# Kernel optimization log

Measured on AMD Instinct MI355X. Metric: run time of the kernel, lower is better.

## Reference

```python
import jax, jax.numpy as jnp
import numpy as np


def _scan(x):
    # x: [B, C, D0, D1, D2] -> [B, 4, C, L] with L = D0*D1*D2
    B, C = x.shape[0], x.shape[1]
    x0 = x.reshape(B, C, -1)                          # row-major flatten of (D0,D1,D2)
    x1 = jnp.swapaxes(x, -2, -1).reshape(B, C, -1)    # swap last two spatial axes then flatten
    x2 = jnp.flip(x0, axis=-1)
    x3 = jnp.flip(x1, axis=-1)
    return jnp.stack([x0, x1, x2, x3], axis=1)        # [B, 4, C, L]


def setup_inputs() -> dict:
    key = jax.random.key(0)
    x = jax.random.normal(key, (2, 96, 32, 32, 32), dtype=jnp.float32)
    return {"x": x}


def reference(x) -> jnp.ndarray:
    # x: [B, C, I, J, K]
    xs_i = _scan(x)                                   # scan over (i, j, k)
    xs_j = _scan(jnp.transpose(x, (0, 1, 3, 4, 2)))   # b c i j k -> b c j k i
    xs_k = _scan(jnp.transpose(x, (0, 1, 4, 2, 3)))   # b c i j k -> b c k i j
    return jnp.concatenate([xs_i, xs_j, xs_k], axis=1)  # [B, 12, C, I*J*K]
```

## Files before the change

### kernel.cpp

```cpp
#include <hip/hip_runtime.h>

#define L 32768
#define NC 96
#define PL 4

typedef float f4 __attribute__((ext_vector_type(4)));


__global__ __launch_bounds__(256) void cross_scan3d(const float* __restrict__ in,
                                                    float* __restrict__ out) {
    __shared__ float lds[PL][32][33];

    const int bx   = blockIdx.x;
    const int type = bx & 1;
    const int bc   = bx >> 1;
    const int b    = bc / NC;
    const int c    = bc % NC;
    const int w0   = blockIdx.y * PL;
    const int tid  = threadIdx.x;

    const int row = tid >> 3;
    const int k4  = tid & 7;

    const f4* src4 = (const f4*)(in + (size_t)bc * L);

    const int sI = type ? 5 : 0;
    const int sT = type ? 4 : 1;
    const int sS = type ? 9 : 8;

    f4* oI  = (f4*)(out + ((size_t)(b*12 + sI    )*NC + c) * L);
    f4* oIf = (f4*)(out + ((size_t)(b*12 + sI + 2)*NC + c) * L);
    f4* oT  = (f4*)(out + ((size_t)(b*12 + sT    )*NC + c) * L);
    f4* oTf = (f4*)(out + ((size_t)(b*12 + sT + 2)*NC + c) * L);
    f4* oS  = (f4*)(out + ((size_t)(b*12 + sS    )*NC + c) * L);
    f4* oSf = (f4*)(out + ((size_t)(b*12 + sS + 2)*NC + c) * L);

    f4 v0, v1, v2, v3;
    #define LADDR(it) (type ? (row*256 + (w0+(it))*8 + k4) : ((w0+(it))*256 + row*8 + k4))
    v0 = src4[LADDR(0)]; v1 = src4[LADDR(1)]; v2 = src4[LADDR(2)]; v3 = src4[LADDR(3)];
    #undef LADDR

    #define STASH(p, V) \
        lds[p][row][k4*4+0] = V.x; lds[p][row][k4*4+1] = V.y; \
        lds[p][row][k4*4+2] = V.z; lds[p][row][k4*4+3] = V.w;
    STASH(0, v0) STASH(1, v1) STASH(2, v2) STASH(3, v3)
    #undef STASH

    __syncthreads();

    #pragma unroll
    for (int p = 0; p < PL; ++p) {
        const int gp = w0 + p;

        f4 a;
        a.x = lds[p][row][k4*4+0];
        a.y = lds[p][row][k4*4+1];
        a.z = lds[p][row][k4*4+2];
        a.w = lds[p][row][k4*4+3];

        f4 t;
        t.x = lds[p][k4*4+0][row];
        t.y = lds[p][k4*4+1][row];
        t.z = lds[p][k4*4+2][row];
        t.w = lds[p][k4*4+3][row];

        const int l0 = gp*256 + row*8 + k4;
        const int lS = row*256 + gp*8 + k4;

        f4 ar = {a.w, a.z, a.y, a.x};
        f4 tr = {t.w, t.z, t.y, t.x};

        __builtin_nontemporal_store(a,  oI  + l0);
        __builtin_nontemporal_store(ar, oIf + (8191 - l0));
        __builtin_nontemporal_store(t,  oT  + l0);
        __builtin_nontemporal_store(tr, oTf + (8191 - l0));
        __builtin_nontemporal_store(t,  oS  + lS);
        __builtin_nontemporal_store(tr, oSf + (8191 - lS));
    }
}

extern "C" void kernel_launch(void* const* d_in, const int* in_sizes, int n_in,
                              void* d_out, int out_size, void* d_ws, size_t ws_size,
                              hipStream_t stream) {
    const float* in = (const float*)d_in[0];
    float* out = (float*)d_out;
    const int bc_count = in_sizes[0] / L;
    dim3 grid(bc_count * 2, 32 / PL);
    cross_scan3d<<<grid, 256, 0, stream>>>(in, out);
}
```

Before: 64.15 us.

## Enlarge per-block tile to 8 slabs and specialize load/store paths per scan type

Each block now stages 8 spatial slabs instead of 4 into LDS, halving the grid's y dimension. The two block types get separate code paths. Type 0 loads contiguous i-slabs and writes the identity and flipped outputs straight from registers. Type 1 loads a j-range across all i and writes its transposed views from LDS. The aim is wider contiguous store runs and fewer, larger blocks. The cost is more LDS per block (about 34KB), which may lower occupancy, plus LDS bank patterns that need checking for each index layout.

```diff
diff --git a/kernel.cpp b/kernel.cpp
--- a/kernel.cpp
+++ b/kernel.cpp
@@ -2,81 +2,132 @@
 
 #define L 32768
 #define NC 96
-#define PL 4
 
 typedef float f4 __attribute__((ext_vector_type(4)));
 
 
 __global__ __launch_bounds__(256) void cross_scan3d(const float* __restrict__ in,
                                                     float* __restrict__ out) {
-    __shared__ float lds[PL][32][33];
+    __shared__ float lds[8480];
 
     const int bx   = blockIdx.x;
     const int type = bx & 1;
     const int bc   = bx >> 1;
     const int b    = bc / NC;
     const int c    = bc % NC;
-    const int w0   = blockIdx.y * PL;
+    const int s0   = blockIdx.y * 8;
     const int tid  = threadIdx.x;
 
-    const int row = tid >> 3;
-    const int k4  = tid & 7;
+    const f4* src4 = (const f4*)(in + (size_t)bc * L);
+    #define OPTR(s) ((f4*)(out + ((size_t)((b)*12 + (s)) * NC + (c)) * L))
+    #define NT(p, v) __builtin_nontemporal_store((v), (p))
 
-    const f4* src4 = (const f4*)(in + (size_t)bc * L);
+    if (type == 0) {
+        f4* o0  = OPTR(0);  f4* o0f = OPTR(2);
+        f4* o1  = OPTR(1);  f4* o1f = OPTR(3);
+        f4* o4  = OPTR(8);  f4* o4f = OPTR(10);
 
-    const int sI = type ? 5 : 0;
-    const int sT = type ? 4 : 1;
-    const int sS = type ? 9 : 8;
+        const int jj = tid >> 3, k4 = tid & 7;
+        #pragma unroll
+        for (int it = 0; it < 8; ++it) {
+            f4 v = src4[(s0 + it) * 256 + tid];
+            float* d = &lds[it * 1057 + jj * 33 + k4 * 4];
+            d[0] = v.x; d[1] = v.y; d[2] = v.z; d[3] = v.w;
+            int o = (s0 + it) * 256 + tid;
+            NT(o0 + o, v);
+            f4 vr = { v.w, v.z, v.y, v.x };
+            NT(o0f + (8191 - o), vr);
+        }
+        __syncthreads();
 
-    f4* oI  = (f4*)(out + ((size_t)(b*12 + sI    )*NC + c) * L);
-    f4* oIf = (f4*)(out + ((size_t)(b*12 + sI + 2)*NC + c) * L);
-    f4* oT  = (f4*)(out + ((size_t)(b*12 + sT    )*NC + c) * L);
-    f4* oTf = (f4*)(out + ((size_t)(b*12 + sT + 2)*NC + c) * L);
-    f4* oS  = (f4*)(out + ((size_t)(b*12 + sS    )*NC + c) * L);
-    f4* oSf = (f4*)(out + ((size_t)(b*12 + sS + 2)*NC + c) * L);
+        const int k_o = tid >> 3, j4 = tid & 7;
+        #pragma unroll
+        for (int it = 0; it < 8; ++it) {
+            f4 t;
+            t.x = lds[it * 1057 + (j4 * 4 + 0) * 33 + k_o];
+            t.y = lds[it * 1057 + (j4 * 4 + 1) * 33 + k_o];
+            t.z = lds[it * 1057 + (j4 * 4 + 2) * 33 + k_o];
+            t.w = lds[it * 1057 + (j4 * 4 + 3) * 33 + k_o];
+            int o = (s0 + it) * 256 + tid;
+            NT(o1 + o, t);
+            f4 tr = { t.w, t.z, t.y, t.x };
+            NT(o1f + (8191 - o), tr);
+        }
 
-    f4 v0, v1, v2, v3;
-    #define LADDR(it) (type ? (row*256 + (w0+(it))*8 + k4) : ((w0+(it))*256 + row*8 + k4))
-    v0 = src4[LADDR(0)]; v1 = src4[LADDR(1)]; v2 = src4[LADDR(2)]; v3 = src4[LADDR(3)];
-    #undef LADDR
+        const int qd = tid >> 6, il = (tid >> 3) & 7, j4b = tid & 7;
+        #pragma unroll
+        for (int n = 0; n < 8; ++n) {
+            int ko = qd * 8 + n;
+            f4 t;
+            t.x = lds[il * 1057 + (j4b * 4 + 0) * 33 + ko];
+            t.y = lds[il * 1057 + (j4b * 4 + 1) * 33 + ko];
+            t.z = lds[il * 1057 + (j4b * 4 + 2) * 33 + ko];
+            t.w = lds[il * 1057 + (j4b * 4 + 3) * 33 + ko];
+            int o = ko * 256 + (s0 + il) * 8 + j4b;
+            NT(o4 + o, t);
+            f4 tr = { t.w, t.z, t.y, t.x };
+            NT(o4f + (8191 - o), tr);
+        }
+    } else {
+        f4* o3  = OPTR(5);  f4* o3f = OPTR(7);
+        f4* o2  = OPTR(4);  f4* o2f = OPTR(6);
+        f4* o5  = OPTR(9);  f4* o5f = OPTR(11);
 
-    #define STASH(p, V) \
-        lds[p][row][k4*4+0] = V.x; lds[p][row][k4*4+1] = V.y; \
-        lds[p][row][k4*4+2] = V.z; lds[p][row][k4*4+3] = V.w;
-    STASH(0, v0) STASH(1, v1) STASH(2, v2) STASH(3, v3)
-    #undef STASH
+        #pragma unroll
+        for (int it = 0; it < 8; ++it) {
+            int i   = it * 4 + (tid >> 6);
+            int rem = tid & 63;
+            f4 v = src4[i * 256 + s0 * 8 + rem];
+            float* d = &lds[i * 265 + (rem >> 3) * 33 + (rem & 7) * 4];
+            d[0] = v.x; d[1] = v.y; d[2] = v.z; d[3] = v.w;
+        }
+        __syncthreads();
 
-    __syncthreads();
+        const int i_o = tid >> 3, k4 = tid & 7;
+        #pragma unroll
+        for (int it = 0; it < 8; ++it) {
+            f4 a;
+            a.x = lds[i_o * 265 + it * 33 + k4 * 4 + 0];
+            a.y = lds[i_o * 265 + it * 33 + k4 * 4 + 1];
+            a.z = lds[i_o * 265 + it * 33 + k4 * 4 + 2];
+            a.w = lds[i_o * 265 + it * 33 + k4 * 4 + 3];
+            int o = (s0 + it) * 256 + tid;
+            NT(o3 + o, a);
+            f4 ar = { a.w, a.z, a.y, a.x };
+            NT(o3f + (8191 - o), ar);
+        }
 
-    #pragma unroll
-    for (int p = 0; p < PL; ++p) {
-        const int gp = w0 + p;
+        const int k_o = tid >> 3, i4 = tid & 7;
+        #pragma unroll
+        for (int it = 0; it < 8; ++it) {
+            f4 t;
+            t.x = lds[(i4 * 4 + 0) * 265 + it * 33 + k_o];
+            t.y = lds[(i4 * 4 + 1) * 265 + it * 33 + k_o];
+            t.z = lds[(i4 * 4 + 2) * 265 + it * 33 + k_o];
+            t.w = lds[(i4 * 4 + 3) * 265 + it * 33 + k_o];
+            int o = (s0 + it) * 256 + tid;
+            NT(o2 + o, t);
+            f4 tr = { t.w, t.z, t.y, t.x };
+            NT(o2f + (8191 - o), tr);
+        }
 
-        f4 a;
-        a.x = lds[p][row][k4*4+0];
-        a.y = lds[p][row][k4*4+1];
-        a.z = lds[p][row][k4*4+2];
-        a.w = lds[p][row][k4*4+3];
-
-        f4 t;
-        t.x = lds[p][k4*4+0][row];
-        t.y = lds[p][k4*4+1][row];
-        t.z = lds[p][k4*4+2][row];
-        t.w = lds[p][k4*4+3][row];
-
-        const int l0 = gp*256 + row*8 + k4;
-        const int lS = row*256 + gp*8 + k4;
-
-        f4 ar = {a.w, a.z, a.y, a.x};
-        f4 tr = {t.w, t.z, t.y, t.x};
-
-        __builtin_nontemporal_store(a,  oI  + l0);
-        __builtin_nontemporal_store(ar, oIf + (8191 - l0));
-        __builtin_nontemporal_store(t,  oT  + l0);
-        __builtin_nontemporal_store(tr, oTf + (8191 - l0));
-        __builtin_nontemporal_store(t,  oS  + lS);
-        __builtin_nontemporal_store(tr, oSf + (8191 - lS));
+        const int qd = tid >> 6, jl = (tid >> 3) & 7, i4b = tid & 7;
+        #pragma unroll
+        for (int n = 0; n < 8; ++n) {
+            int ko = qd * 8 + n;
+            f4 t;
+            t.x = lds[(i4b * 4 + 0) * 265 + jl * 33 + ko];
+            t.y = lds[(i4b * 4 + 1) * 265 + jl * 33 + ko];
+            t.z = lds[(i4b * 4 + 2) * 265 + jl * 33 + ko];
+            t.w = lds[(i4b * 4 + 3) * 265 + jl * 33 + ko];
+            int o = ko * 256 + (s0 + jl) * 8 + i4b;
+            NT(o5 + o, t);
+            f4 tr = { t.w, t.z, t.y, t.x };
+            NT(o5f + (8191 - o), tr);
+        }
     }
+    #undef OPTR
+    #undef NT
 }
 
 extern "C" void kernel_launch(void* const* d_in, const int* in_sizes, int n_in,
@@ -85,6 +136,6 @@
     const float* in = (const float*)d_in[0];
     float* out = (float*)d_out;
     const int bc_count = in_sizes[0] / L;
-    dim3 grid(bc_count * 2, 32 / PL);
+    dim3 grid(bc_count * 2, 4);
     cross_scan3d<<<grid, 256, 0, stream>>>(in, out);
 }
```

Result: no change. 63.92 us (-0.4%).

## Process whole channel volume per block in LDS, emitting all twelve scans

Applied to the files above, without the earlier changes.

Each 1024-thread block now loads an entire 32x32x32 channel volume into padded dynamic LDS and writes all six permutations plus their flips. This means the input is read once per channel instead of once per pass type, and the identity copy is written straight from registers during the load. The trade-off is a grid of only one block per (batch, channel) with roughly 135 KB of LDS each. That limits occupancy to one block per CU and leaves some CUs idle, which could reduce store bandwidth.

```diff
diff --git a/kernel.cpp b/kernel.cpp
--- a/kernel.cpp
+++ b/kernel.cpp
@@ -2,81 +2,119 @@
 
 #define L 32768
 #define NC 96
-#define PL 4
+#define LDS_FLOATS (32 * 1057)
+#define LDS_BYTES  (LDS_FLOATS * 4)
 
 typedef float f4 __attribute__((ext_vector_type(4)));
 
 
-__global__ __launch_bounds__(256) void cross_scan3d(const float* __restrict__ in,
-                                                    float* __restrict__ out) {
-    __shared__ float lds[PL][32][33];
+__global__ __launch_bounds__(1024) void cross_scan3d(const float* __restrict__ in,
+                                                     float* __restrict__ out) {
+    extern __shared__ float lds[];
 
-    const int bx   = blockIdx.x;
-    const int type = bx & 1;
-    const int bc   = bx >> 1;
-    const int b    = bc / NC;
-    const int c    = bc % NC;
-    const int w0   = blockIdx.y * PL;
-    const int tid  = threadIdx.x;
-
-    const int row = tid >> 3;
-    const int k4  = tid & 7;
+    const int bc  = blockIdx.x;
+    const int b   = bc / NC;
+    const int c   = bc % NC;
+    const int tid = threadIdx.x;
 
     const f4* src4 = (const f4*)(in + (size_t)bc * L);
+    #define OPTR(s) ((f4*)(out + ((size_t)((b)*12 + (s)) * NC + (c)) * L))
+    #define NT(p, v) __builtin_nontemporal_store((v), (p))
+    #define A(i, j, k) ((i) * 1057 + (j) * 33 + (k))
 
-    const int sI = type ? 5 : 0;
-    const int sT = type ? 4 : 1;
-    const int sS = type ? 9 : 8;
+    f4* o0 = OPTR(0);  f4* o0f = OPTR(2);
+    f4* o1 = OPTR(1);  f4* o1f = OPTR(3);
+    f4* o2 = OPTR(4);  f4* o2f = OPTR(6);
+    f4* o3 = OPTR(5);  f4* o3f = OPTR(7);
+    f4* o4 = OPTR(8);  f4* o4f = OPTR(10);
+    f4* o5 = OPTR(9);  f4* o5f = OPTR(11);
 
-    f4* oI  = (f4*)(out + ((size_t)(b*12 + sI    )*NC + c) * L);
-    f4* oIf = (f4*)(out + ((size_t)(b*12 + sI + 2)*NC + c) * L);
-    f4* oT  = (f4*)(out + ((size_t)(b*12 + sT    )*NC + c) * L);
-    f4* oTf = (f4*)(out + ((size_t)(b*12 + sT + 2)*NC + c) * L);
-    f4* oS  = (f4*)(out + ((size_t)(b*12 + sS    )*NC + c) * L);
-    f4* oSf = (f4*)(out + ((size_t)(b*12 + sS + 2)*NC + c) * L);
-
-    f4 v0, v1, v2, v3;
-    #define LADDR(it) (type ? (row*256 + (w0+(it))*8 + k4) : ((w0+(it))*256 + row*8 + k4))
-    v0 = src4[LADDR(0)]; v1 = src4[LADDR(1)]; v2 = src4[LADDR(2)]; v3 = src4[LADDR(3)];
-    #undef LADDR
-
-    #define STASH(p, V) \
-        lds[p][row][k4*4+0] = V.x; lds[p][row][k4*4+1] = V.y; \
-        lds[p][row][k4*4+2] = V.z; lds[p][row][k4*4+3] = V.w;
-    STASH(0, v0) STASH(1, v1) STASH(2, v2) STASH(3, v3)
-    #undef STASH
-
+    #pragma unroll
+    for (int it = 0; it < 8; ++it) {
+        int t = it * 1024 + tid;
+        f4 v = src4[t];
+        int i = t >> 8, j = (t >> 3) & 31, k4 = t & 7;
+        float* d = &lds[A(i, j, k4 * 4)];
+        d[0] = v.x; d[1] = v.y; d[2] = v.z; d[3] = v.w;
+        NT(o0 + t, v);
+        f4 vr = { v.w, v.z, v.y, v.x };
+        NT(o0f + (8191 - t), vr);
+    }
     __syncthreads();
 
     #pragma unroll
-    for (int p = 0; p < PL; ++p) {
-        const int gp = w0 + p;
+    for (int it = 0; it < 8; ++it) {
+        int t = it * 1024 + tid;
+        int i = t >> 8, k = (t >> 3) & 31, j4 = t & 7;
+        f4 v;
+        v.x = lds[A(i, j4 * 4 + 0, k)];
+        v.y = lds[A(i, j4 * 4 + 1, k)];
+        v.z = lds[A(i, j4 * 4 + 2, k)];
+        v.w = lds[A(i, j4 * 4 + 3, k)];
+        NT(o1 + t, v);
+        f4 vr = { v.w, v.z, v.y, v.x };
+        NT(o1f + (8191 - t), vr);
+    }
 
-        f4 a;
-        a.x = lds[p][row][k4*4+0];
-        a.y = lds[p][row][k4*4+1];
-        a.z = lds[p][row][k4*4+2];
-        a.w = lds[p][row][k4*4+3];
+    #pragma unroll
+    for (int it = 0; it < 8; ++it) {
+        int t = it * 1024 + tid;
+        int j = t >> 8, i = (t >> 3) & 31, k4 = t & 7;
+        f4 v;
+        v.x = lds[A(i, j, k4 * 4 + 0)];
+        v.y = lds[A(i, j, k4 * 4 + 1)];
+        v.z = lds[A(i, j, k4 * 4 + 2)];
+        v.w = lds[A(i, j, k4 * 4 + 3)];
+        NT(o3 + t, v);
+        f4 vr = { v.w, v.z, v.y, v.x };
+        NT(o3f + (8191 - t), vr);
+    }
 
-        f4 t;
-        t.x = lds[p][k4*4+0][row];
-        t.y = lds[p][k4*4+1][row];
-        t.z = lds[p][k4*4+2][row];
-        t.w = lds[p][k4*4+3][row];
+    #pragma unroll
+    for (int it = 0; it < 8; ++it) {
+        int t = it * 1024 + tid;
+        int j = t >> 8, k = (t >> 3) & 31, i4 = t & 7;
+        f4 v;
+        v.x = lds[A(i4 * 4 + 0, j, k)];
+        v.y = lds[A(i4 * 4 + 1, j, k)];
+        v.z = lds[A(i4 * 4 + 2, j, k)];
+        v.w = lds[A(i4 * 4 + 3, j, k)];
+        NT(o2 + t, v);
+        f4 vr = { v.w, v.z, v.y, v.x };
+        NT(o2f + (8191 - t), vr);
+    }
 
-        const int l0 = gp*256 + row*8 + k4;
-        const int lS = row*256 + gp*8 + k4;
+    #pragma unroll
+    for (int it = 0; it < 8; ++it) {
+        int t = it * 1024 + tid;
+        int k = t >> 8, i = (t >> 3) & 31, j4 = t & 7;
+        f4 v;
+        v.x = lds[A(i, j4 * 4 + 0, k)];
+        v.y = lds[A(i, j4 * 4 + 1, k)];
+        v.z = lds[A(i, j4 * 4 + 2, k)];
+        v.w = lds[A(i, j4 * 4 + 3, k)];
+        NT(o4 + t, v);
+        f4 vr = { v.w, v.z, v.y, v.x };
+        NT(o4f + (8191 - t), vr);
+    }
 
-        f4 ar = {a.w, a.z, a.y, a.x};
-        f4 tr = {t.w, t.z, t.y, t.x};
+    #pragma unroll
+    for (int it = 0; it < 8; ++it) {
+        int t = it * 1024 + tid;
+        int k = t >> 8, j = (t >> 3) & 31, i4 = t & 7;
+        f4 v;
+        v.x = lds[A(i4 * 4 + 0, j, k)];
+        v.y = lds[A(i4 * 4 + 1, j, k)];
+        v.z = lds[A(i4 * 4 + 2, j, k)];
+        v.w = lds[A(i4 * 4 + 3, j, k)];
+        NT(o5 + t, v);
+        f4 vr = { v.w, v.z, v.y, v.x };
+        NT(o5f + (8191 - t), vr);
+    }
 
-        __builtin_nontemporal_store(a,  oI  + l0);
-        __builtin_nontemporal_store(ar, oIf + (8191 - l0));
-        __builtin_nontemporal_store(t,  oT  + l0);
-        __builtin_nontemporal_store(tr, oTf + (8191 - l0));
-        __builtin_nontemporal_store(t,  oS  + lS);
-        __builtin_nontemporal_store(tr, oSf + (8191 - lS));
-    }
+    #undef OPTR
+    #undef NT
+    #undef A
 }
 
 extern "C" void kernel_launch(void* const* d_in, const int* in_sizes, int n_in,
@@ -85,6 +123,9 @@
     const float* in = (const float*)d_in[0];
     float* out = (float*)d_out;
     const int bc_count = in_sizes[0] / L;
-    dim3 grid(bc_count * 2, 32 / PL);
-    cross_scan3d<<<grid, 256, 0, stream>>>(in, out);
+
+    (void)hipFuncSetAttribute((const void*)cross_scan3d,
+                              hipFuncAttributeMaxDynamicSharedMemorySize, LDS_BYTES);
+
+    cross_scan3d<<<dim3(bc_count), 1024, LDS_BYTES, stream>>>(in, out);
 }
```

Result: faster. 61.73 us (-3.8%).
